# Performance work log

Hardware: AMD Instinct MI355X
Metric: run time of the kernel (lower is better)

The kernel has to match this reference:

```python
import jax, jax.numpy as jnp
import numpy as np

NEG_INF = -1e18  # fp32 masking constant used by the original module


def setup_inputs() -> dict:
    key0 = jax.random.key(0)
    kq, kk, kv, km, ke = jax.random.split(key0, 5)
    B, L, H, C = 2, 2048, 16, 64
    query = jax.random.normal(kq, (B, L, H, C), dtype=jnp.float32)
    key = jax.random.normal(kk, (B, L, H, C), dtype=jnp.float32)
    value = jax.random.normal(kv, (B, L, H, C), dtype=jnp.float32)
    mask = jax.random.randint(km, (B, L, L), 0, 2).astype(jnp.bool_)
    edge_scores = jax.random.normal(ke, (1, H, L, L), dtype=jnp.float32)
    return {"query": query, "key": key, "value": value, "mask": mask,
            "edge_scores": edge_scores}


def _masked_softmax(att_score, mask):
    # mask: True -> keep, False -> masked. Fill with -1e18 (fp32 path),
    # softmax, then multiply by mask (post-softmax zeroing), as in original.
    s = jnp.where(mask, att_score, NEG_INF)
    w = jax.nn.softmax(s, axis=-1)
    return w * mask.astype(w.dtype)


def reference(query, key, value, mask, edge_scores):
    # layout 'NTK': query/key/value (B, L, H, C); mask (B, Lq, Lm)
    scale = jnp.sqrt(jnp.asarray(query.shape[-1], dtype=query.dtype))
    # scores: (B, H, Lq, Lm)
    scores = jnp.einsum('binc,bjnc->bnij', query, key)
    scores = scores + edge_scores
    attn_weights = _masked_softmax(scores / scale, mask[:, None, :, :])
    # dropout rate is 0.0 -> identity
    # context: (B, Lq, H, Cv) -> (B, Lq, H*Cv)
    context = jnp.einsum('bnij,bjnc->binc', attn_weights, value)
    B, Lq = context.shape[0], context.shape[1]
    context_vec = context.reshape(B, Lq, -1)
    return (context_vec, scores, attn_weights)
```

## Files before the change

### kernel.cpp

```cpp
#include <hip/hip_runtime.h>


typedef __attribute__((ext_vector_type(8))) short bf16x8;
typedef __attribute__((ext_vector_type(4))) float f32x4;
typedef __attribute__((ext_vector_type(4))) int   i32x4;

#define LQ 2048
#define NH 16
#define CD 64

__device__ inline short f2bf(float x) {
    union { float f; unsigned u; } v; v.f = x;
    unsigned r = v.u + 0x7FFFu + ((v.u >> 16) & 1u);
    return (short)(r >> 16);
}

__device__ inline bf16x8 pack8(f32x4 a, f32x4 b) {
    bf16x8 r;
    r[0] = f2bf(a[0]); r[1] = f2bf(a[1]); r[2] = f2bf(a[2]); r[3] = f2bf(a[3]);
    r[4] = f2bf(b[0]); r[5] = f2bf(b[1]); r[6] = f2bf(b[2]); r[7] = f2bf(b[3]);
    return r;
}

__device__ inline void lds_barrier() {
    asm volatile("s_waitcnt lgkmcnt(0)" ::: "memory");
    __builtin_amdgcn_s_barrier();
}

#define SWZ(base, row, bytecol) \
    ((char*)(base) + ((row) * 128) + ((bytecol) ^ (((row) & 7) << 4)))

__global__ __launch_bounds__(256, 4)
void k_attn(const float* __restrict__ q, const float* __restrict__ kk,
            const float* __restrict__ v, const int* __restrict__ mask,
            const float* __restrict__ edge,
            float* __restrict__ sc, float* __restrict__ attn,
            float* __restrict__ ctx)
{
    __shared__ short KsD[2][64][64];
    __shared__ short Vt[64][64];
    __shared__ short Wt[4][16][64];

    const int flat = blockIdx.x;
    const int L = (flat & 7) * 128 + (flat >> 3);
    const int z = L >> 5;
    const int i0 = (L & 31) * 64;
    const int b = z & 1, h = z >> 1;

    const int tid = threadIdx.x;
    const int r = tid >> 2, seg = (tid & 3) * 16;
    const int rgrp = tid >> 4, c4 = tid & 15;
    const int wave = tid >> 6, lane = tid & 63;
    const int quad = lane >> 4, mm = lane & 15;

    char* const ks0 = (char*)&KsD[0][0][0];
    char* const ks1 = (char*)&KsD[1][0][0];
    char* const vtb = (char*)&Vt[0][0];
    char* const wtb = (char*)&Wt[wave][0][0];

    const int gi = i0 + wave * 16 + mm;
    const float* qp = q + ((size_t)((b * LQ + gi) * NH + h)) * CD;
    bf16x8 qa0 = pack8(*(const f32x4*)(qp + quad * 8), *(const f32x4*)(qp + quad * 8 + 4));
    bf16x8 qa1 = pack8(*(const f32x4*)(qp + 32 + quad * 8), *(const f32x4*)(qp + 32 + quad * 8 + 4));

    const float* erow = edge + ((size_t)(h * LQ + gi)) * LQ;
    const int*   mrow = mask + ((size_t)(b * LQ + gi)) * LQ;
    const size_t srow = ((size_t)((b * NH + h) * LQ + gi)) * LQ;

    const float* kbase = kk + ((size_t)((b * LQ + r) * NH + h)) * CD + seg;
    const float* vbase = v  + ((size_t)((b * LQ + rgrp * 4) * NH + h)) * CD + c4 * 4;
    const size_t kstep = (size_t)64 * NH * CD;

    f32x4 ev[4]; i32x4 mv[4];
    #pragma unroll
    for (int jt = 0; jt < 4; ++jt) {
        ev[jt] = *(const f32x4*)(erow + jt * 16 + quad * 4);
        mv[jt] = *(const i32x4*)(mrow + jt * 16 + quad * 4);
    }

    f32x4 kr[4];
    #pragma unroll
    for (int u = 0; u < 4; ++u) kr[u] = ((const f32x4*)kbase)[u];
    #pragma unroll
    for (int u = 0; u < 4; ++u)
        *(short4*)SWZ(ks0, r, 2 * seg + 8 * u) =
            make_short4(f2bf(kr[u][0]), f2bf(kr[u][1]), f2bf(kr[u][2]), f2bf(kr[u][3]));
    #pragma unroll
    for (int u = 0; u < 4; ++u) kr[u] = ((const f32x4*)(kbase + kstep))[u];
    lds_barrier();

    float lacc = 0.f;
    for (int jb = 0; jb < 32; ++jb) {
        const int j0 = jb * 64;
        char* const kscur = (jb & 1) ? ks1 : ks0;
        char* const ksnxt = (jb & 1) ? ks0 : ks1;
        if (jb < 31) {
            #pragma unroll
            for (int u = 0; u < 4; ++u)
                *(short4*)SWZ(ksnxt, r, 2 * seg + 8 * u) =
                    make_short4(f2bf(kr[u][0]), f2bf(kr[u][1]), f2bf(kr[u][2]), f2bf(kr[u][3]));
            if (jb < 30) {
                const float* kp = kbase + kstep * (jb + 2);
                #pragma unroll
                for (int u = 0; u < 4; ++u) kr[u] = ((const f32x4*)kp)[u];
            }
        }
        f32x4 acc[4];
        #pragma unroll
        for (int jt = 0; jt < 4; ++jt) {
            bf16x8 k0 = *(const bf16x8*)SWZ(kscur, jt * 16 + mm, 16 * quad);
            bf16x8 k1 = *(const bf16x8*)SWZ(kscur, jt * 16 + mm, 64 + 16 * quad);
            f32x4 a = {0.f, 0.f, 0.f, 0.f};
            a = __builtin_amdgcn_mfma_f32_16x16x32_bf16(k0, qa0, a, 0, 0, 0);
            a = __builtin_amdgcn_mfma_f32_16x16x32_bf16(k1, qa1, a, 0, 0, 0);
            acc[jt] = a;
        }
        #pragma unroll
        for (int jt = 0; jt < 4; ++jt) {
            f32x4 s4 = acc[jt] + ev[jt];
            __builtin_nontemporal_store(s4, (f32x4*)(sc + srow + j0 + jt * 16 + quad * 4));
            lacc += (mv[jt][0] ? __expf(s4[0] * 0.125f) : 0.f)
                  + (mv[jt][1] ? __expf(s4[1] * 0.125f) : 0.f)
                  + (mv[jt][2] ? __expf(s4[2] * 0.125f) : 0.f)
                  + (mv[jt][3] ? __expf(s4[3] * 0.125f) : 0.f);
        }
        if (jb < 31) {
            #pragma unroll
            for (int jt = 0; jt < 4; ++jt) {
                ev[jt] = *(const f32x4*)(erow + j0 + 64 + jt * 16 + quad * 4);
                mv[jt] = *(const i32x4*)(mrow + j0 + 64 + jt * 16 + quad * 4);
            }
        }
        lds_barrier();
    }

    lacc += __shfl_xor(lacc, 16, 64);
    lacc += __shfl_xor(lacc, 32, 64);
    const float inv = (lacc > 0.f) ? 1.f / lacc : 0.f;

    f32x4 vr[4];
    #pragma unroll
    for (int u = 0; u < 4; ++u) kr[u] = ((const f32x4*)kbase)[u];
    #pragma unroll
    for (int t = 0; t < 4; ++t) vr[t] = *(const f32x4*)(vbase + t * (NH * CD));
    #pragma unroll
    for (int jt = 0; jt < 4; ++jt) {
        ev[jt] = *(const f32x4*)(erow + jt * 16 + quad * 4);
        mv[jt] = *(const i32x4*)(mrow + jt * 16 + quad * 4);
    }
    f32x4 cacc[4] = { {0,0,0,0}, {0,0,0,0}, {0,0,0,0}, {0,0,0,0} };

    for (int jb = 0; jb < 32; ++jb) {
        const int j0 = jb * 64;
        #pragma unroll
        for (int u = 0; u < 4; ++u)
            *(short4*)SWZ(ks0, r, 2 * seg + 8 * u) =
                make_short4(f2bf(kr[u][0]), f2bf(kr[u][1]), f2bf(kr[u][2]), f2bf(kr[u][3]));
        #pragma unroll
        for (int cs = 0; cs < 4; ++cs)
            *(short4*)SWZ(vtb, c4 * 4 + cs, 8 * rgrp) =
                make_short4(f2bf(vr[0][cs]), f2bf(vr[1][cs]), f2bf(vr[2][cs]), f2bf(vr[3][cs]));
        lds_barrier();

        f32x4 acc[4];
        #pragma unroll
        for (int jt = 0; jt < 4; ++jt) {
            bf16x8 k0 = *(const bf16x8*)SWZ(ks0, jt * 16 + mm, 16 * quad);
            bf16x8 k1 = *(const bf16x8*)SWZ(ks0, jt * 16 + mm, 64 + 16 * quad);
            f32x4 a = {0.f, 0.f, 0.f, 0.f};
            a = __builtin_amdgcn_mfma_f32_16x16x32_bf16(k0, qa0, a, 0, 0, 0);
            a = __builtin_amdgcn_mfma_f32_16x16x32_bf16(k1, qa1, a, 0, 0, 0);
            acc[jt] = a;
        }

        if (jb < 31) {
            const float* kp = kbase + kstep * (jb + 1);
            const float* vp = vbase + kstep * (jb + 1);
            #pragma unroll
            for (int u = 0; u < 4; ++u) kr[u] = ((const f32x4*)kp)[u];
            #pragma unroll
            for (int t = 0; t < 4; ++t) vr[t] = *(const f32x4*)(vp + t * (NH * CD));
        }

        #pragma unroll
        for (int jt = 0; jt < 4; ++jt) {
            f32x4 s4 = acc[jt] + ev[jt];
            f32x4 w;
            w[0] = mv[jt][0] ? __expf(s4[0] * 0.125f) * inv : 0.f;
            w[1] = mv[jt][1] ? __expf(s4[1] * 0.125f) * inv : 0.f;
            w[2] = mv[jt][2] ? __expf(s4[2] * 0.125f) * inv : 0.f;
            w[3] = mv[jt][3] ? __expf(s4[3] * 0.125f) * inv : 0.f;
            __builtin_nontemporal_store(w, (f32x4*)(attn + srow + j0 + jt * 16 + quad * 4));
            *(short4*)SWZ(wtb, mm, 32 * jt + 8 * quad) =
                make_short4(f2bf(w[0]), f2bf(w[1]), f2bf(w[2]), f2bf(w[3]));
        }

        if (jb < 31) {
            #pragma unroll
            for (int jt = 0; jt < 4; ++jt) {
                ev[jt] = *(const f32x4*)(erow + j0 + 64 + jt * 16 + quad * 4);
                mv[jt] = *(const i32x4*)(mrow + j0 + 64 + jt * 16 + quad * 4);
            }
        }

        #pragma unroll
        for (int kt = 0; kt < 2; ++kt) {
            bf16x8 aw = *(const bf16x8*)SWZ(wtb, mm, 64 * kt + 16 * quad);
            #pragma unroll
            for (int nt = 0; nt < 4; ++nt) {
                bf16x8 bb = *(const bf16x8*)SWZ(vtb, nt * 16 + mm, 64 * kt + 16 * quad);
                cacc[nt] = __builtin_amdgcn_mfma_f32_16x16x32_bf16(aw, bb, cacc[nt], 0, 0, 0);
            }
        }
        lds_barrier();
    }

    const int irow = i0 + wave * 16 + quad * 4;
    #pragma unroll
    for (int nt = 0; nt < 4; ++nt) {
        const int c = nt * 16 + mm;
        #pragma unroll
        for (int reg = 0; reg < 4; ++reg) {
            const int i = irow + reg;
            __builtin_nontemporal_store(cacc[nt][reg],
                ctx + ((size_t)(b * LQ + i)) * (NH * CD) + h * CD + c);
        }
    }
}

extern "C" void kernel_launch(void* const* d_in, const int* in_sizes, int n_in,
                              void* d_out, int out_size, void* d_ws, size_t ws_size,
                              hipStream_t stream) {
    const float* q    = (const float*)d_in[0];
    const float* k    = (const float*)d_in[1];
    const float* v    = (const float*)d_in[2];
    const int*   mask = (const int*)d_in[3];
    const float* edge = (const float*)d_in[4];

    float* out = (float*)d_out;
    float* ctx = out;
    float* sc  = out + 4194304;
    float* at  = sc + 134217728;

    k_attn<<<dim3(1024), 256, 0, stream>>>(q, k, v, mask, edge, sc, at, ctx);
}
```

Measured before the change: 1.672 ms.

## Double-buffer K and V tiles in second pass and drop nontemporal stores

The second (softmax-weight and PV) pass now double-buffers K and V tiles in LDS, writing the next tile and prefetching two tiles ahead. This removes one barrier per iteration and hides global load latency, matching the first pass. The shared memory is merged into one 40 KB buffer, up from 32 KB, which may reduce occupancy. Nontemporal stores for scores, attention weights and context are replaced with ordinary stores, which changes cache behaviour for the large output writes.

```diff
diff --git a/kernel.cpp b/kernel.cpp
--- a/kernel.cpp
+++ b/kernel.cpp
@@ -8,6 +8,7 @@
 #define LQ 2048
 #define NH 16
 #define CD 64
+#define NHC (NH*CD)
 
 __device__ inline short f2bf(float x) {
     union { float f; unsigned u; } v; v.f = x;
@@ -29,6 +30,7 @@
 
 #define SWZ(base, row, bytecol) \
     ((char*)(base) + ((row) * 128) + ((bytecol) ^ (((row) & 7) << 4)))
+
 
 __global__ __launch_bounds__(256, 4)
 void k_attn(const float* __restrict__ q, const float* __restrict__ kk,
@@ -37,9 +39,7 @@
             float* __restrict__ sc, float* __restrict__ attn,
             float* __restrict__ ctx)
 {
-    __shared__ short KsD[2][64][64];
-    __shared__ short Vt[64][64];
-    __shared__ short Wt[4][16][64];
+    __shared__ __align__(16) char lds[40960];
 
     const int flat = blockIdx.x;
     const int L = (flat & 7) * 128 + (flat >> 3);
@@ -53,10 +53,7 @@
     const int wave = tid >> 6, lane = tid & 63;
     const int quad = lane >> 4, mm = lane & 15;
 
-    char* const ks0 = (char*)&KsD[0][0][0];
-    char* const ks1 = (char*)&KsD[1][0][0];
-    char* const vtb = (char*)&Vt[0][0];
-    char* const wtb = (char*)&Wt[wave][0][0];
+    char* const wtb = lds + 32768 + wave * 2048;
 
     const int gi = i0 + wave * 16 + mm;
     const float* qp = q + ((size_t)((b * LQ + gi) * NH + h)) * CD;
@@ -69,7 +66,7 @@
 
     const float* kbase = kk + ((size_t)((b * LQ + r) * NH + h)) * CD + seg;
     const float* vbase = v  + ((size_t)((b * LQ + rgrp * 4) * NH + h)) * CD + c4 * 4;
-    const size_t kstep = (size_t)64 * NH * CD;
+    const size_t kstep = (size_t)64 * NHC;
 
     f32x4 ev[4]; i32x4 mv[4];
     #pragma unroll
@@ -83,7 +80,7 @@
     for (int u = 0; u < 4; ++u) kr[u] = ((const f32x4*)kbase)[u];
     #pragma unroll
     for (int u = 0; u < 4; ++u)
-        *(short4*)SWZ(ks0, r, 2 * seg + 8 * u) =
+        *(short4*)SWZ(lds, r, 2 * seg + 8 * u) =
             make_short4(f2bf(kr[u][0]), f2bf(kr[u][1]), f2bf(kr[u][2]), f2bf(kr[u][3]));
     #pragma unroll
     for (int u = 0; u < 4; ++u) kr[u] = ((const f32x4*)(kbase + kstep))[u];
@@ -92,12 +89,12 @@
     float lacc = 0.f;
     for (int jb = 0; jb < 32; ++jb) {
         const int j0 = jb * 64;
-        char* const kscur = (jb & 1) ? ks1 : ks0;
-        char* const ksnxt = (jb & 1) ? ks0 : ks1;
-        if (jb < 31) {
+        const int cur = jb & 1;
+        if (jb < 31) {
+            char* kn = lds + (cur ^ 1) * 8192;
             #pragma unroll
             for (int u = 0; u < 4; ++u)
-                *(short4*)SWZ(ksnxt, r, 2 * seg + 8 * u) =
+                *(short4*)SWZ(kn, r, 2 * seg + 8 * u) =
                     make_short4(f2bf(kr[u][0]), f2bf(kr[u][1]), f2bf(kr[u][2]), f2bf(kr[u][3]));
             if (jb < 30) {
                 const float* kp = kbase + kstep * (jb + 2);
@@ -105,11 +102,12 @@
                 for (int u = 0; u < 4; ++u) kr[u] = ((const f32x4*)kp)[u];
             }
         }
+        char* const kb = lds + cur * 8192;
         f32x4 acc[4];
         #pragma unroll
         for (int jt = 0; jt < 4; ++jt) {
-            bf16x8 k0 = *(const bf16x8*)SWZ(kscur, jt * 16 + mm, 16 * quad);
-            bf16x8 k1 = *(const bf16x8*)SWZ(kscur, jt * 16 + mm, 64 + 16 * quad);
+            bf16x8 k0 = *(const bf16x8*)SWZ(kb, jt * 16 + mm, 16 * quad);
+            bf16x8 k1 = *(const bf16x8*)SWZ(kb, jt * 16 + mm, 64 + 16 * quad);
             f32x4 a = {0.f, 0.f, 0.f, 0.f};
             a = __builtin_amdgcn_mfma_f32_16x16x32_bf16(k0, qa0, a, 0, 0, 0);
             a = __builtin_amdgcn_mfma_f32_16x16x32_bf16(k1, qa1, a, 0, 0, 0);
@@ -118,7 +116,7 @@
         #pragma unroll
         for (int jt = 0; jt < 4; ++jt) {
             f32x4 s4 = acc[jt] + ev[jt];
-            __builtin_nontemporal_store(s4, (f32x4*)(sc + srow + j0 + jt * 16 + quad * 4));
+            *(f32x4*)(sc + srow + j0 + jt * 16 + quad * 4) = s4;
             lacc += (mv[jt][0] ? __expf(s4[0] * 0.125f) : 0.f)
                   + (mv[jt][1] ? __expf(s4[1] * 0.125f) : 0.f)
                   + (mv[jt][2] ? __expf(s4[2] * 0.125f) : 0.f)
@@ -142,44 +140,66 @@
     #pragma unroll
     for (int u = 0; u < 4; ++u) kr[u] = ((const f32x4*)kbase)[u];
     #pragma unroll
-    for (int t = 0; t < 4; ++t) vr[t] = *(const f32x4*)(vbase + t * (NH * CD));
+    for (int t = 0; t < 4; ++t) vr[t] = *(const f32x4*)(vbase + t * NHC);
     #pragma unroll
     for (int jt = 0; jt < 4; ++jt) {
         ev[jt] = *(const f32x4*)(erow + jt * 16 + quad * 4);
         mv[jt] = *(const i32x4*)(mrow + jt * 16 + quad * 4);
     }
+    #pragma unroll
+    for (int u = 0; u < 4; ++u)
+        *(short4*)SWZ(lds, r, 2 * seg + 8 * u) =
+            make_short4(f2bf(kr[u][0]), f2bf(kr[u][1]), f2bf(kr[u][2]), f2bf(kr[u][3]));
+    #pragma unroll
+    for (int cs = 0; cs < 4; ++cs)
+        *(short4*)SWZ(lds + 16384, c4 * 4 + cs, 8 * rgrp) =
+            make_short4(f2bf(vr[0][cs]), f2bf(vr[1][cs]), f2bf(vr[2][cs]), f2bf(vr[3][cs]));
+    {
+        const float* kp = kbase + kstep;
+        const float* vp = vbase + kstep;
+        #pragma unroll
+        for (int u = 0; u < 4; ++u) kr[u] = ((const f32x4*)kp)[u];
+        #pragma unroll
+        for (int t = 0; t < 4; ++t) vr[t] = *(const f32x4*)(vp + t * NHC);
+    }
+    lds_barrier();
+
     f32x4 cacc[4] = { {0,0,0,0}, {0,0,0,0}, {0,0,0,0}, {0,0,0,0} };
 
     for (int jb = 0; jb < 32; ++jb) {
         const int j0 = jb * 64;
-        #pragma unroll
-        for (int u = 0; u < 4; ++u)
-            *(short4*)SWZ(ks0, r, 2 * seg + 8 * u) =
-                make_short4(f2bf(kr[u][0]), f2bf(kr[u][1]), f2bf(kr[u][2]), f2bf(kr[u][3]));
-        #pragma unroll
-        for (int cs = 0; cs < 4; ++cs)
-            *(short4*)SWZ(vtb, c4 * 4 + cs, 8 * rgrp) =
-                make_short4(f2bf(vr[0][cs]), f2bf(vr[1][cs]), f2bf(vr[2][cs]), f2bf(vr[3][cs]));
-        lds_barrier();
-
+        const int cur = jb & 1;
+        if (jb < 31) {
+            char* kn = lds + (cur ^ 1) * 8192;
+            char* vn = lds + 16384 + (cur ^ 1) * 8192;
+            #pragma unroll
+            for (int u = 0; u < 4; ++u)
+                *(short4*)SWZ(kn, r, 2 * seg + 8 * u) =
+                    make_short4(f2bf(kr[u][0]), f2bf(kr[u][1]), f2bf(kr[u][2]), f2bf(kr[u][3]));
+            #pragma unroll
+            for (int cs = 0; cs < 4; ++cs)
+                *(short4*)SWZ(vn, c4 * 4 + cs, 8 * rgrp) =
+                    make_short4(f2bf(vr[0][cs]), f2bf(vr[1][cs]), f2bf(vr[2][cs]), f2bf(vr[3][cs]));
+            if (jb < 30) {
+                const float* kp = kbase + kstep * (jb + 2);
+                const float* vp = vbase + kstep * (jb + 2);
+                #pragma unroll
+                for (int u = 0; u < 4; ++u) kr[u] = ((const f32x4*)kp)[u];
+                #pragma unroll
+                for (int t = 0; t < 4; ++t) vr[t] = *(const f32x4*)(vp + t * NHC);
+            }
+        }
+
+        char* const kb = lds + cur * 8192;
         f32x4 acc[4];
         #pragma unroll
         for (int jt = 0; jt < 4; ++jt) {
-            bf16x8 k0 = *(const bf16x8*)SWZ(ks0, jt * 16 + mm, 16 * quad);
-            bf16x8 k1 = *(const bf16x8*)SWZ(ks0, jt * 16 + mm, 64 + 16 * quad);
+            bf16x8 k0 = *(const bf16x8*)SWZ(kb, jt * 16 + mm, 16 * quad);
+            bf16x8 k1 = *(const bf16x8*)SWZ(kb, jt * 16 + mm, 64 + 16 * quad);
             f32x4 a = {0.f, 0.f, 0.f, 0.f};
             a = __builtin_amdgcn_mfma_f32_16x16x32_bf16(k0, qa0, a, 0, 0, 0);
             a = __builtin_amdgcn_mfma_f32_16x16x32_bf16(k1, qa1, a, 0, 0, 0);
             acc[jt] = a;
-        }
-
-        if (jb < 31) {
-            const float* kp = kbase + kstep * (jb + 1);
-            const float* vp = vbase + kstep * (jb + 1);
-            #pragma unroll
-            for (int u = 0; u < 4; ++u) kr[u] = ((const f32x4*)kp)[u];
-            #pragma unroll
-            for (int t = 0; t < 4; ++t) vr[t] = *(const f32x4*)(vp + t * (NH * CD));
         }
 
         #pragma unroll
@@ -190,7 +210,7 @@
             w[1] = mv[jt][1] ? __expf(s4[1] * 0.125f) * inv : 0.f;
             w[2] = mv[jt][2] ? __expf(s4[2] * 0.125f) * inv : 0.f;
             w[3] = mv[jt][3] ? __expf(s4[3] * 0.125f) * inv : 0.f;
-            __builtin_nontemporal_store(w, (f32x4*)(attn + srow + j0 + jt * 16 + quad * 4));
+            *(f32x4*)(attn + srow + j0 + jt * 16 + quad * 4) = w;
             *(short4*)SWZ(wtb, mm, 32 * jt + 8 * quad) =
                 make_short4(f2bf(w[0]), f2bf(w[1]), f2bf(w[2]), f2bf(w[3]));
         }
@@ -203,13 +223,14 @@
             }
         }
 
+        char* const vb = lds + 16384 + cur * 8192;
         #pragma unroll
         for (int kt = 0; kt < 2; ++kt) {
             bf16x8 aw = *(const bf16x8*)SWZ(wtb, mm, 64 * kt + 16 * quad);
             #pragma unroll
             for (int nt = 0; nt < 4; ++nt) {
-                bf16x8 bb = *(const bf16x8*)SWZ(vtb, nt * 16 + mm, 64 * kt + 16 * quad);
-                cacc[nt] = __builtin_amdgcn_mfma_f32_16x16x32_bf16(aw, bb, cacc[nt], 0, 0, 0);
+                bf16x8 bbv = *(const bf16x8*)SWZ(vb, nt * 16 + mm, 64 * kt + 16 * quad);
+                cacc[nt] = __builtin_amdgcn_mfma_f32_16x16x32_bf16(aw, bbv, cacc[nt], 0, 0, 0);
             }
         }
         lds_barrier();
@@ -222,8 +243,7 @@
         #pragma unroll
         for (int reg = 0; reg < 4; ++reg) {
             const int i = irow + reg;
-            __builtin_nontemporal_store(cacc[nt][reg],
-                ctx + ((size_t)(b * LQ + i)) * (NH * CD) + h * CD + c);
+            ctx[((size_t)(b * LQ + i)) * NHC + h * CD + c] = cacc[nt][reg];
         }
     }
 }
```

After: 1.662 ms. No clear change (-0.6%).
